# Kernel optimization log

Measured on AMD Instinct MI355X. Metric: run time of the kernel, lower is better.

Reference implementation:

```python
import jax, jax.numpy as jnp
import numpy as np

B, L, D = 4, 4096, 1024
N_HEADS = 16
HEAD_SIZE = D // N_HEADS  # 64


def setup_inputs() -> dict:
    key = jax.random.key(0)
    k_x, k_w, k_m = jax.random.split(key, 3)
    x = jax.random.normal(k_x, (B, L, D), dtype=jnp.float32)
    # nn.Linear(D, 3*head_size, bias=False): weight (3*hs, D); store transposed (D, 3*hs)
    W_qkv = jax.random.normal(k_w, (D, 3 * HEAD_SIZE), dtype=jnp.float32) * (D ** -0.5)
    attn_mask = jax.random.randint(k_m, (B, L), 0, 2).astype(jnp.bool_)
    return {"x": x, "attn_mask": attn_mask, "W_qkv": W_qkv}


def reference(x, attn_mask, W_qkv):
    # x: (B, L, D); W_qkv: (D, 3*hs); attn_mask: (B, L) True = attend
    qkv = x @ W_qkv                                # (B, L, 3*hs)
    q, k, v = jnp.split(qkv, 3, axis=-1)           # each (B, L, hs)
    scale = HEAD_SIZE ** -0.5
    scores = jnp.einsum('bqd,bkd->bqk', q, k) * scale   # (B, L, L)
    neg_inf = jnp.finfo(scores.dtype).min
    scores = jnp.where(attn_mask[:, None, :], scores, neg_inf)
    weights = jax.nn.softmax(scores, axis=-1)      # (B, L, L)
    out = jnp.einsum('bqk,bkd->bqd', weights, v)   # (B, L, hs)
    return out
```

## Files before the change

kernel.cpp:

```cpp
#include <hip/hip_runtime.h>

typedef __bf16 bf16_t;
typedef __bf16 bf16x8 __attribute__((ext_vector_type(8)));
typedef __bf16 bf16x4 __attribute__((ext_vector_type(4)));
typedef float  f32x4  __attribute__((ext_vector_type(4)));
struct uint4_t { unsigned x, y, z, w; };

#define B_  4
#define L_  4096
#define D_  1024
#define HS  64
#define NQ  192
#define SCL2E 0.1803368801111204f
#define MFMA16 __builtin_amdgcn_mfma_f32_16x16x32_bf16

__global__ __launch_bounds__(256) void pack_w_kernel(const void* __restrict__ Win,
                                                     const unsigned char* __restrict__ mask,
                                                     const unsigned short* __restrict__ xw,
                                                     bf16_t* __restrict__ Wtp,
                                                     int* __restrict__ flags) {
    __shared__ int c1, c23, cbad;
    int tid = threadIdx.x;
    if (tid == 0) { c1 = 0; c23 = 0; cbad = 0; }
    __syncthreads();
    uint4_t m[4];
#pragma unroll
    for (int i = 0; i < 4; ++i)
        m[i] = *(const uint4_t*)(mask + tid * 16 + i * 4096);
    int a = 0, bc = 0;
#pragma unroll
    for (int i = 0; i < 4; ++i) {
        const unsigned* w = (const unsigned*)&m[i];
#pragma unroll
        for (int j = 0; j < 4; ++j) {
            if (w[j] & 0x0000ff00u) a++;
            if (w[j] & 0xffff0000u) bc++;
        }
    }
    uint4_t xm = *(const uint4_t*)(xw + tid * 8);
    int bad = 0;
    const unsigned* xwv = (const unsigned*)&xm;
#pragma unroll
    for (int j = 0; j < 4; ++j)
#pragma unroll
        for (int h = 0; h < 2; ++h) {
            unsigned s = (xwv[j] >> (16 * h)) & 0xFFFFu;
            unsigned e = (s >> 7) & 0xFF;
            if (e > 150 || (e < 90 && e != 0)) bad++;
        }
    if (a)   atomicAdd(&c1, a);
    if (bc)  atomicAdd(&c23, bc);
    if (bad) atomicAdd(&cbad, bad);
    __syncthreads();
    int f32 = (cbad >= 64) ? 1 : 0;
    if (blockIdx.x == 0 && tid == 0) {
        flags[0] = (c1 > 0) ? 1 : ((c23 > 0) ? 2 : 0);
        flags[1] = f32;
    }

    int idx = blockIdx.x * 256 + tid;
    int lane = idx & 63;
    int t    = (idx >> 6) & 3;
    int kc   = (idx >> 8) & 31;
    int ct   = idx >> 13;
    int n  = ct * 64 + t * 16 + (lane & 15);
    int k0 = kc * 32 + (lane >> 4) * 8;
    bf16x8 v;
#pragma unroll
    for (int j = 0; j < 8; ++j) {
        if (f32) v[j] = (bf16_t)(((const float*)Win)[(k0 + j) * NQ + n]);
        else     v[j] = ((const bf16_t*)Win)[(k0 + j) * NQ + n];
    }
    *(bf16x8*)(Wtp + (size_t)idx * 8) = v;
}

__global__ __launch_bounds__(256, 2) void qkv_gemm_kernel(const void* __restrict__ xin,
                                                          const int* __restrict__ flags,
                                                          const bf16_t* __restrict__ Wtp,
                                                          bf16_t* __restrict__ Qb,
                                                          bf16_t* __restrict__ Kb,
                                                          bf16_t* __restrict__ Vt) {
    __shared__ __align__(16) bf16_t xs[32 * 520];
    __shared__ __align__(16) bf16_t sqk[32 * 136];
    __shared__ __align__(16) bf16_t sv[64 * 40];

    int tid = threadIdx.x;
    int wave = tid >> 6, lane = tid & 63, quad = lane >> 4, l16 = lane & 15;
    int rg = wave & 1, ch = wave >> 1;
    int m0 = blockIdx.x * 32;
    int xf = flags[1];

    f32x4 acc[6] = {};
    bf16x8 Ba[6], Bb[6];

    auto stage = [&](int h) {
        bf16x8 tmp[8];
#pragma unroll
        for (int j = 0; j < 8; ++j) {
            int c = tid + j * 256;
            int row = c >> 6, off = (c & 63) * 8;
            if (xf) {
                const float* xp = (const float*)xin + (size_t)(m0 + row) * D_ + h * 512 + off;
                f32x4 lo = *(const f32x4*)xp, hi = *(const f32x4*)(xp + 4);
                tmp[j][0] = (bf16_t)lo[0]; tmp[j][1] = (bf16_t)lo[1];
                tmp[j][2] = (bf16_t)lo[2]; tmp[j][3] = (bf16_t)lo[3];
                tmp[j][4] = (bf16_t)hi[0]; tmp[j][5] = (bf16_t)hi[1];
                tmp[j][6] = (bf16_t)hi[2]; tmp[j][7] = (bf16_t)hi[3];
            } else {
                tmp[j] = *(const bf16x8*)((const bf16_t*)xin + (size_t)(m0 + row) * D_ + h * 512 + off);
            }
        }
#pragma unroll
        for (int j = 0; j < 8; ++j) {
            int c = tid + j * 256;
            int row = c >> 6, off = (c & 63) * 8;
            *(bf16x8*)&xs[row * 520 + off] = tmp[j];
        }
    };
    auto loadB6 = [&](int ks, bf16x8* Bv) {
#pragma unroll
        for (int i = 0; i < 6; ++i) {
            int st = ch * 6 + i, ct2 = st >> 2, tt = st & 3;
            Bv[i] = *(const bf16x8*)(Wtp + ((size_t)(ct2 * 32 + ks) * 4 + tt) * 512 + lane * 8);
        }
    };
    auto compute6 = [&](int ks, const bf16x8* Bv) {
        bf16x8 A = *(const bf16x8*)&xs[(rg * 16 + l16) * 520 + (ks & 15) * 32 + quad * 8];
#pragma unroll
        for (int i = 0; i < 6; ++i)
            acc[i] = MFMA16(A, Bv[i], acc[i], 0, 0, 0);
    };

    stage(0);
    loadB6(0, Ba);
    __syncthreads();
#pragma unroll
    for (int half = 0; half < 2; ++half) {
        int base = half * 16;
        for (int m = 0; m < 16; m += 2) {
            int ks = base + m;
            loadB6(ks + 1, Bb);
            compute6(ks, Ba);
            loadB6(ks + 2 <= 31 ? ks + 2 : 31, Ba);
            compute6(ks + 1, Bb);
        }
        if (half == 0) {
            __syncthreads();
            stage(1);
            __syncthreads();
        }
    }

    int rowb = rg * 16 + quad * 4;
#pragma unroll
    for (int i = 0; i < 6; ++i) {
        int col = ch * 96 + i * 16 + l16;
#pragma unroll
        for (int r = 0; r < 4; ++r) {
            bf16_t hv = (bf16_t)acc[i][r];
            if (col < 128) sqk[(rowb + r) * 136 + col] = hv;
            else           sv[(col - 128) * 40 + rowb + r] = hv;
        }
    }
    __syncthreads();

    int bb = m0 >> 12, l0 = m0 & 4095;
#pragma unroll
    for (int it = 0; it < 2; ++it) {
        int c = tid + it * 256;
        int row = c >> 4, off = (c & 15) * 8;
        bf16x8 v = *(const bf16x8*)&sqk[row * 136 + off];
        if (off < 64) *(bf16x8*)(Qb + (size_t)(bb * L_ + l0 + row) * HS + off) = v;
        else          *(bf16x8*)(Kb + (size_t)(bb * L_ + l0 + row) * HS + off - 64) = v;
    }
    {
        int d = tid >> 2, off = (tid & 3) * 8;
        bf16x8 v = *(const bf16x8*)&sv[d * 40 + off];
        *(bf16x8*)(Vt + (size_t)(bb * HS + d) * L_ + l0 + off) = v;
    }
}

template<int NSPLIT>
__global__ __launch_bounds__(256, 4) void attn_kernel(const bf16_t* __restrict__ Qb,
                                                      const bf16_t* __restrict__ Kb,
                                                      const bf16_t* __restrict__ Vt,
                                                      const void* __restrict__ maskp,
                                                      const int* __restrict__ flags,
                                                      float* __restrict__ Opart,
                                                      float* __restrict__ lpart,
                                                      void* __restrict__ outv) {
    constexpr int KCH = L_ / NSPLIT;
    constexpr int NIT = KCH / 64;
    __shared__ __align__(16) bf16_t ktile[2][64 * 72];
    __shared__ __align__(16) bf16_t plds[4][32 * 72];
    __shared__ float mb[KCH];

    int tid = threadIdx.x, wave = tid >> 6, lane = tid & 63;
    int quad = lane >> 4, l16 = lane & 15;
    int grp = blockIdx.x % (B_ * NSPLIT);
    int qt  = blockIdx.x / (B_ * NSPLIT);
    int s = grp / B_, b = grp % B_;
    int q0 = qt * 128;
    int kbase = s * KCH;

    const float NEGINF = -__builtin_inff();
    int mkind = flags[0];
    if (mkind == 1) {
        const unsigned char* mp = (const unsigned char*)maskp + b * L_ + kbase;
        for (int i = tid; i < KCH; i += 256) mb[i] = mp[i] ? 0.0f : NEGINF;
    } else if (mkind == 2) {
        const float* mp = (const float*)maskp + b * L_ + kbase;
        for (int i = tid; i < KCH; i += 256) mb[i] = (mp[i] != 0.0f) ? 0.0f : NEGINF;
    } else {
        const int* mp = (const int*)maskp + b * L_ + kbase;
        for (int i = tid; i < KCH; i += 256) mb[i] = mp[i] ? 0.0f : NEGINF;
    }

    bf16x8 aQ[2][2];
#pragma unroll
    for (int rg = 0; rg < 2; ++rg) {
        const bf16_t* qp = Qb + (size_t)(b * L_ + q0 + wave * 32 + rg * 16 + l16) * HS + quad * 8;
        aQ[rg][0] = *(const bf16x8*)qp;
        aQ[rg][1] = *(const bf16x8*)(qp + 32);
    }
    bf16x8 ones;
#pragma unroll
    for (int j = 0; j < 8; ++j) ones[j] = (bf16_t)1.0f;

    const bf16_t* Kbase = Kb + (size_t)b * L_ * HS;
    const bf16_t* Vbase = Vt + (size_t)b * HS * L_;

    f32x4 O[2][4] = {};
    f32x4 O5[2] = {};
    bf16_t* pw = &plds[wave][0];
    bf16x8 kr[2];

    auto kstage_load = [&](int t) {
#pragma unroll
        for (int j = 0; j < 2; ++j) {
            int c = tid + j * 256;
            int row = c >> 3, off = (c & 7) * 8;
            kr[j] = *(const bf16x8*)(Kbase + (size_t)(kbase + t * 64 + row) * HS + off);
        }
    };
    auto kstage_store = [&](int buf) {
#pragma unroll
        for (int j = 0; j < 2; ++j) {
            int c = tid + j * 256;
            int row = c >> 3, off = (c & 7) * 8;
            *(bf16x8*)&ktile[buf][row * 72 + off] = kr[j];
        }
    };

    kstage_load(0);
    kstage_store(0);
    __syncthreads();

    for (int t = 0; t < NIT; ++t) {
        int kb = kbase + t * 64;
        bool more = (t + 1 < NIT);
        if (more) kstage_load(t + 1);

        bf16x8 V0[4];
#pragma unroll
        for (int nt = 0; nt < 4; ++nt)
            V0[nt] = *(const bf16x8*)(Vbase + (size_t)(nt * 16 + l16) * L_ + kb + quad * 8);

        const bf16_t* kl = &ktile[t & 1][0];
#pragma unroll
        for (int h = 0; h < 2; ++h) {
            f32x4 sc[2][2];
#pragma unroll
            for (int s2 = 0; s2 < 2; ++s2) {
                int st = h * 2 + s2;
                bf16x8 kb0 = *(const bf16x8*)&kl[(st * 16 + l16) * 72 + quad * 8];
                bf16x8 kb1 = *(const bf16x8*)&kl[(st * 16 + l16) * 72 + 32 + quad * 8];
#pragma unroll
                for (int rg = 0; rg < 2; ++rg) {
                    f32x4 t0 = {};
                    t0 = MFMA16(aQ[rg][0], kb0, t0, 0, 0, 0);
                    t0 = MFMA16(aQ[rg][1], kb1, t0, 0, 0, 0);
                    sc[rg][s2] = t0;
                }
            }
#pragma unroll
            for (int s2 = 0; s2 < 2; ++s2) {
                int st = h * 2 + s2;
                float bl = mb[t * 64 + st * 16 + l16];
#pragma unroll
                for (int rg = 0; rg < 2; ++rg)
#pragma unroll
                    for (int r = 0; r < 4; ++r) {
                        float p = exp2f(fmaf(sc[rg][s2][r], SCL2E, bl));
                        pw[(rg * 16 + quad * 4 + r) * 72 + st * 16 + l16] = (bf16_t)p;
                    }
            }
        }

#pragma unroll
        for (int rg = 0; rg < 2; ++rg) {
            bf16x8 aP = *(const bf16x8*)&pw[(rg * 16 + l16) * 72 + quad * 8];
#pragma unroll
            for (int nt = 0; nt < 4; ++nt)
                O[rg][nt] = MFMA16(aP, V0[nt], O[rg][nt], 0, 0, 0);
            O5[rg] = MFMA16(aP, ones, O5[rg], 0, 0, 0);
        }
        bf16x8 V1[4];
#pragma unroll
        for (int nt = 0; nt < 4; ++nt)
            V1[nt] = *(const bf16x8*)(Vbase + (size_t)(nt * 16 + l16) * L_ + kb + 32 + quad * 8);
#pragma unroll
        for (int rg = 0; rg < 2; ++rg) {
            bf16x8 aP = *(const bf16x8*)&pw[(rg * 16 + l16) * 72 + 32 + quad * 8];
#pragma unroll
            for (int nt = 0; nt < 4; ++nt)
                O[rg][nt] = MFMA16(aP, V1[nt], O[rg][nt], 0, 0, 0);
            O5[rg] = MFMA16(aP, ones, O5[rg], 0, 0, 0);
        }

        if (more) kstage_store((t + 1) & 1);
        __syncthreads();
    }

    int of32 = flags[1];
#pragma unroll
    for (int rg = 0; rg < 2; ++rg)
#pragma unroll
        for (int r = 0; r < 4; ++r) {
            float sm = O5[rg][r];
            int row = q0 + wave * 32 + rg * 16 + quad * 4 + r;
            if (NSPLIT == 1) {
                float inv = 1.0f / sm;
                size_t base = (size_t)(b * L_ + row) * HS;
                if (of32) {
                    float* op = (float*)outv + base;
#pragma unroll
                    for (int nt = 0; nt < 4; ++nt) op[nt * 16 + l16] = O[rg][nt][r] * inv;
                } else {
                    bf16_t* op = (bf16_t*)outv + base;
#pragma unroll
                    for (int nt = 0; nt < 4; ++nt) op[nt * 16 + l16] = (bf16_t)(O[rg][nt][r] * inv);
                }
            } else {
                float* op = Opart + (size_t)s * (B_ * L_ * HS) + (size_t)(b * L_ + row) * HS;
#pragma unroll
                for (int nt = 0; nt < 4; ++nt) op[nt * 16 + l16] = O[rg][nt][r];
                if (l16 == 0) lpart[(size_t)s * (B_ * L_) + b * L_ + row] = sm;
            }
        }
}

__global__ __launch_bounds__(256) void reduce_kernel(const float* __restrict__ Opart,
                                                     const float* __restrict__ lpart,
                                                     const int* __restrict__ flags,
                                                     void* __restrict__ outv,
                                                     int nsplit) {
    int i4 = (blockIdx.x * 256 + threadIdx.x) * 4;
    int row = i4 >> 6;
    f32x4 acc = {};
    float lsum = 0.f;
    for (int s = 0; s < nsplit; ++s) {
        acc  += *(const f32x4*)&Opart[(size_t)s * (B_ * L_ * HS) + i4];
        lsum += lpart[(size_t)s * (B_ * L_) + row];
    }
    float inv = 1.0f / lsum;
    if (flags[1]) {
        f32x4 r = { acc[0] * inv, acc[1] * inv, acc[2] * inv, acc[3] * inv };
        *(f32x4*)&((float*)outv)[i4] = r;
    } else {
        bf16x4 r;
#pragma unroll
        for (int j = 0; j < 4; ++j) r[j] = (bf16_t)(acc[j] * inv);
        *(bf16x4*)&((bf16_t*)outv)[i4] = r;
    }
}

extern "C" void kernel_launch(void* const* d_in, const int* in_sizes, int n_in,
                              void* d_out, int out_size, void* d_ws, size_t ws_size,
                              hipStream_t stream) {
    (void)in_sizes; (void)n_in; (void)out_size;
    const void* x    = d_in[0];
    const void* mask = d_in[1];
    const void* W    = d_in[2];

    char* ws = (char*)d_ws;
    bf16_t* Qb    = (bf16_t*)(ws);
    bf16_t* Kb    = (bf16_t*)(ws + (2u << 20));
    bf16_t* Vt    = (bf16_t*)(ws + (4u << 20));
    bf16_t* Wtp   = (bf16_t*)(ws + (6u << 20));
    int*    flags = (int*)   (ws + (6u << 20) + (512u << 10));
    float*  Opart = (float*) (ws + (7u << 20));

    auto need = [](int ns) -> size_t {
        return (7u << 20) + (size_t)ns * (B_ * L_ * HS * 4)
                          + (size_t)ns * (B_ * L_ * 4) + 4096;
    };
    int nsplit = (ws_size >= need(8)) ? 8 : (ws_size >= need(4)) ? 4 : 1;
    float* lpart = (float*)(ws + (7u << 20) + (size_t)nsplit * (B_ * L_ * HS * 4));

    pack_w_kernel<<<96, 256, 0, stream>>>(W, (const unsigned char*)mask,
                                          (const unsigned short*)x, Wtp, flags);
    qkv_gemm_kernel<<<512, 256, 0, stream>>>(x, flags, Wtp, Qb, Kb, Vt);
    if (nsplit == 8) {
        attn_kernel<8><<<32 * B_ * 8, 256, 0, stream>>>(Qb, Kb, Vt, mask, flags,
                                                        Opart, lpart, d_out);
        reduce_kernel<<<(B_ * L_ * HS) / 1024, 256, 0, stream>>>(Opart, lpart, flags,
                                                                 d_out, 8);
    } else if (nsplit == 4) {
        attn_kernel<4><<<32 * B_ * 4, 256, 0, stream>>>(Qb, Kb, Vt, mask, flags,
                                                        Opart, lpart, d_out);
        reduce_kernel<<<(B_ * L_ * HS) / 1024, 256, 0, stream>>>(Opart, lpart, flags,
                                                                 d_out, 4);
    } else {
        attn_kernel<1><<<32 * B_, 256, 0, stream>>>(Qb, Kb, Vt, mask, flags,
                                                    Opart, lpart, d_out);
    }
}
```

Before: 168.8 us.

## Pre-pack K/V in MFMA fragment layout, fold scale and mask, use 32x32 MFMA

The QKV GEMM epilogue now pre-scales Q by scale*log2e, multiplies V by a 0/1 mask, and writes K and V in MFMA-fragment-packed order. The attention kernel switches to 32x32x16 MFMA with S computed transposed. This lets P go straight from registers to the PV MFMA via permlane32 swaps instead of an LDS round trip. Masking is done by zeroing V and by a denominator MFMA against the mask vector, and K is staged with global_load_lds. The aim is to remove the LDS traffic for P, the per-element mask add and scale FMA, and strided V loads. The cost is more register pressure (occupancy hint drops from 4 to 3) and reliance on the softmax running without max subtraction.

```diff
diff --git a/kernel.cpp b/kernel.cpp
--- a/kernel.cpp
+++ b/kernel.cpp
@@ -3,7 +3,9 @@
 typedef __bf16 bf16_t;
 typedef __bf16 bf16x8 __attribute__((ext_vector_type(8)));
 typedef __bf16 bf16x4 __attribute__((ext_vector_type(4)));
+typedef __bf16 bf16x2 __attribute__((ext_vector_type(2)));
 typedef float  f32x4  __attribute__((ext_vector_type(4)));
+typedef float  f32x16 __attribute__((ext_vector_type(16)));
 struct uint4_t { unsigned x, y, z, w; };
 
 #define B_  4
@@ -13,12 +15,32 @@
 #define NQ  192
 #define SCL2E 0.1803368801111204f
 #define MFMA16 __builtin_amdgcn_mfma_f32_16x16x32_bf16
+#define MFMA32 __builtin_amdgcn_mfma_f32_32x32x16_bf16
+
+#if defined(__has_builtin)
+# if __has_builtin(__builtin_amdgcn_global_load_lds)
+#  define HAS_GLL 1
+# endif
+#endif
+#ifndef HAS_GLL
+# define HAS_GLL 0
+#endif
+
+static __device__ __forceinline__ unsigned pk_bf16(float a, float b) {
+    union { bf16x2 v; unsigned u; } x;
+    x.v[0] = (bf16_t)a; x.v[1] = (bf16_t)b;
+    return x.u;
+}
+static __device__ __forceinline__ void swap32(unsigned& x, unsigned& y) {
+    asm("v_permlane32_swap_b32 %0, %1" : "+v"(x), "+v"(y));
+}
 
 __global__ __launch_bounds__(256) void pack_w_kernel(const void* __restrict__ Win,
                                                      const unsigned char* __restrict__ mask,
                                                      const unsigned short* __restrict__ xw,
                                                      bf16_t* __restrict__ Wtp,
-                                                     int* __restrict__ flags) {
+                                                     int* __restrict__ flags,
+                                                     bf16_t* __restrict__ m01) {
     __shared__ int c1, c23, cbad;
     int tid = threadIdx.x;
     if (tid == 0) { c1 = 0; c23 = 0; cbad = 0; }
@@ -53,12 +75,22 @@
     if (bad) atomicAdd(&cbad, bad);
     __syncthreads();
     int f32 = (cbad >= 64) ? 1 : 0;
+    int kind = (c1 > 0) ? 1 : ((c23 > 0) ? 2 : 0);
     if (blockIdx.x == 0 && tid == 0) {
-        flags[0] = (c1 > 0) ? 1 : ((c23 > 0) ? 2 : 0);
+        flags[0] = kind;
         flags[1] = f32;
     }
 
     int idx = blockIdx.x * 256 + tid;
+
+    if (idx < B_ * L_) {
+        bool mv;
+        if (kind == 1)      mv = mask[idx] != 0;
+        else if (kind == 2) mv = ((const float*)mask)[idx] != 0.0f;
+        else                mv = ((const int*)mask)[idx] != 0;
+        m01[idx] = (bf16_t)(mv ? 1.0f : 0.0f);
+    }
+
     int lane = idx & 63;
     int t    = (idx >> 6) & 3;
     int kc   = (idx >> 8) & 31;
@@ -77,9 +109,10 @@
 __global__ __launch_bounds__(256, 2) void qkv_gemm_kernel(const void* __restrict__ xin,
                                                           const int* __restrict__ flags,
                                                           const bf16_t* __restrict__ Wtp,
+                                                          const bf16_t* __restrict__ m01p,
                                                           bf16_t* __restrict__ Qb,
-                                                          bf16_t* __restrict__ Kb,
-                                                          bf16_t* __restrict__ Vt) {
+                                                          bf16_t* __restrict__ Kp,
+                                                          bf16_t* __restrict__ Vp) {
     __shared__ __align__(16) bf16_t xs[32 * 520];
     __shared__ __align__(16) bf16_t sqk[32 * 136];
     __shared__ __align__(16) bf16_t sv[64 * 40];
@@ -157,7 +190,9 @@
         int col = ch * 96 + i * 16 + l16;
 #pragma unroll
         for (int r = 0; r < 4; ++r) {
-            bf16_t hv = (bf16_t)acc[i][r];
+            float av = acc[i][r];
+            if (col < 64) av *= SCL2E;
+            bf16_t hv = (bf16_t)av;
             if (col < 128) sqk[(rowb + r) * 136 + col] = hv;
             else           sv[(col - 128) * 40 + rowb + r] = hv;
         }
@@ -165,189 +200,155 @@
     __syncthreads();
 
     int bb = m0 >> 12, l0 = m0 & 4095;
-#pragma unroll
-    for (int it = 0; it < 2; ++it) {
-        int c = tid + it * 256;
-        int row = c >> 4, off = (c & 15) * 8;
+    int t64 = l0 >> 6, stile = (l0 >> 5) & 1, ctop = (l0 >> 4) & 2;
+    {
+        int row = tid >> 3, off = (tid & 7) * 8;
         bf16x8 v = *(const bf16x8*)&sqk[row * 136 + off];
-        if (off < 64) *(bf16x8*)(Qb + (size_t)(bb * L_ + l0 + row) * HS + off) = v;
-        else          *(bf16x8*)(Kb + (size_t)(bb * L_ + l0 + row) * HS + off - 64) = v;
+        *(bf16x8*)(Qb + (size_t)(m0 + row) * HS + off) = v;
     }
     {
-        int d = tid >> 2, off = (tid & 3) * 8;
-        bf16x8 v = *(const bf16x8*)&sv[d * 40 + off];
-        *(bf16x8*)(Vt + (size_t)(bb * HS + d) * L_ + l0 + off) = v;
+        int chk = tid >> 6, ln = tid & 63;
+        bf16x8 v = *(const bf16x8*)&sqk[(tid & 31) * 136 + 64 + chk * 16 + ((tid >> 5) & 1) * 8];
+        *(bf16x8*)(Kp + (size_t)bb * (L_ * HS) +
+                   ((((size_t)t64 * 2 + stile) * 4 + chk) * 64 + ln) * 8) = v;
+    }
+    {
+        int dt = tid >> 7, chL = (tid >> 6) & 1, ln = tid & 63;
+        int hi2 = (tid >> 5) & 1, d31 = tid & 31;
+        bf16x8 v  = *(const bf16x8*)&sv[(dt * 32 + d31) * 40 + chL * 16 + hi2 * 8];
+        bf16x8 mm = *(const bf16x8*)(m01p + (size_t)m0 + chL * 16 + hi2 * 8);
+        bf16x8 o;
+#pragma unroll
+        for (int j = 0; j < 8; ++j) o[j] = (bf16_t)((float)v[j] * (float)mm[j]);
+        *(bf16x8*)(Vp + (size_t)bb * (L_ * HS) +
+                   ((((size_t)t64 * 2 + dt) * 4 + ctop + chL) * 64 + ln) * 8) = o;
     }
 }
 
 template<int NSPLIT>
-__global__ __launch_bounds__(256, 4) void attn_kernel(const bf16_t* __restrict__ Qb,
-                                                      const bf16_t* __restrict__ Kb,
-                                                      const bf16_t* __restrict__ Vt,
-                                                      const void* __restrict__ maskp,
+__global__ __launch_bounds__(256, 3) void attn_kernel(const bf16_t* __restrict__ Qb,
+                                                      const bf16_t* __restrict__ Kp,
+                                                      const bf16_t* __restrict__ Vp,
+                                                      const bf16_t* __restrict__ m01p,
                                                       const int* __restrict__ flags,
                                                       float* __restrict__ Opart,
                                                       float* __restrict__ lpart,
                                                       void* __restrict__ outv) {
     constexpr int KCH = L_ / NSPLIT;
     constexpr int NIT = KCH / 64;
-    __shared__ __align__(16) bf16_t ktile[2][64 * 72];
-    __shared__ __align__(16) bf16_t plds[4][32 * 72];
-    __shared__ float mb[KCH];
+    __shared__ __align__(16) bf16_t ktile[2][4096];
 
     int tid = threadIdx.x, wave = tid >> 6, lane = tid & 63;
-    int quad = lane >> 4, l16 = lane & 15;
+    int hi = lane >> 5, l31 = lane & 31;
     int grp = blockIdx.x % (B_ * NSPLIT);
     int qt  = blockIdx.x / (B_ * NSPLIT);
-    int s = grp / B_, b = grp % B_;
-    int q0 = qt * 128;
-    int kbase = s * KCH;
-
-    const float NEGINF = -__builtin_inff();
-    int mkind = flags[0];
-    if (mkind == 1) {
-        const unsigned char* mp = (const unsigned char*)maskp + b * L_ + kbase;
-        for (int i = tid; i < KCH; i += 256) mb[i] = mp[i] ? 0.0f : NEGINF;
-    } else if (mkind == 2) {
-        const float* mp = (const float*)maskp + b * L_ + kbase;
-        for (int i = tid; i < KCH; i += 256) mb[i] = (mp[i] != 0.0f) ? 0.0f : NEGINF;
+    int sp = grp / B_, b = grp % B_;
+    int q0 = qt * 128 + wave * 32;
+    int t64base = sp * NIT;
+
+    const bf16_t* KpB = Kp + (size_t)b * (L_ * HS);
+    const bf16_t* VpB = Vp + (size_t)b * (L_ * HS);
+    const bf16_t* mB  = m01p + (size_t)b * L_ + sp * KCH;
+
+    bf16x8 Qf[4];
+    {
+        const bf16_t* qp = Qb + (size_t)(b * L_ + q0 + l31) * HS + hi * 8;
+#pragma unroll
+        for (int c = 0; c < 4; ++c) Qf[c] = *(const bf16x8*)(qp + c * 16);
+    }
+
+    f32x16 O0 = {}, O1 = {}, den = {};
+
+    auto stage = [&](int buf, int t64) {
+        const bf16_t* src = KpB + (size_t)t64 * 4096 + tid * 8;
+        bf16_t* dst = &ktile[buf][tid * 8];
+#if HAS_GLL
+#pragma unroll
+        for (int j = 0; j < 2; ++j)
+            __builtin_amdgcn_global_load_lds(
+                (const __attribute__((address_space(1))) unsigned*)(src + j * 2048),
+                (__attribute__((address_space(3))) unsigned*)(dst + j * 2048), 16, 0, 0);
+#else
+#pragma unroll
+        for (int j = 0; j < 2; ++j)
+            *(bf16x8*)(dst + j * 2048) = *(const bf16x8*)(src + j * 2048);
+#endif
+    };
+
+    stage(0, t64base);
+    __syncthreads();
+
+    for (int t = 0; t < NIT; ++t) {
+        int cur = t & 1;
+        if (t + 1 < NIT) stage(cur ^ 1, t64base + t + 1);
+        const bf16_t* kl = &ktile[cur][0];
+        const bf16_t* vt = VpB + (size_t)(t64base + t) * 4096;
+        const bf16_t* mt = mB + t * 64;
+
+#pragma unroll
+        for (int st = 0; st < 2; ++st) {
+            f32x16 S = {};
+#pragma unroll
+            for (int c = 0; c < 4; ++c) {
+                bf16x8 Kf = *(const bf16x8*)&kl[((st * 4 + c) * 64 + lane) * 8];
+                S = MFMA32(Kf, Qf[c], S, 0, 0, 0);
+            }
+#pragma unroll
+            for (int r = 0; r < 16; ++r) S[r] = exp2f(S[r]);
+#pragma unroll
+            for (int cc = 0; cc < 2; ++cc) {
+                int chk = st * 2 + cc;
+                unsigned w0 = pk_bf16(S[cc * 8 + 0], S[cc * 8 + 1]);
+                unsigned w1 = pk_bf16(S[cc * 8 + 2], S[cc * 8 + 3]);
+                unsigned w2 = pk_bf16(S[cc * 8 + 4], S[cc * 8 + 5]);
+                unsigned w3 = pk_bf16(S[cc * 8 + 6], S[cc * 8 + 7]);
+                swap32(w0, w2);
+                swap32(w1, w3);
+                union { unsigned u[4]; bf16x8 v; } P;
+                P.u[0] = w0; P.u[1] = w1; P.u[2] = w2; P.u[3] = w3;
+                bf16x8 V0 = *(const bf16x8*)&vt[((0 * 4 + chk) * 64 + lane) * 8];
+                bf16x8 V1 = *(const bf16x8*)&vt[((1 * 4 + chk) * 64 + lane) * 8];
+                bf16x8 Mf = *(const bf16x8*)(mt + chk * 16 + hi * 8);
+                O0  = MFMA32(P.v, V0, O0, 0, 0, 0);
+                O1  = MFMA32(P.v, V1, O1, 0, 0, 0);
+                den = MFMA32(P.v, Mf, den, 0, 0, 0);
+            }
+        }
+        __syncthreads();
+    }
+
+    if (NSPLIT == 1) {
+        int of32 = flags[1];
+#pragma unroll
+        for (int r = 0; r < 16; ++r) {
+            int qr = (r & 3) + 8 * (r >> 2) + 4 * hi;
+            float inv = 1.0f / den[r];
+            size_t base = (size_t)(b * L_ + q0 + qr) * HS;
+            if (of32) {
+                float* op = (float*)outv + base;
+                op[l31]      = O0[r] * inv;
+                op[32 + l31] = O1[r] * inv;
+            } else {
+                bf16_t* op = (bf16_t*)outv + base;
+                op[l31]      = (bf16_t)(O0[r] * inv);
+                op[32 + l31] = (bf16_t)(O1[r] * inv);
+            }
+        }
     } else {
-        const int* mp = (const int*)maskp + b * L_ + kbase;
-        for (int i = tid; i < KCH; i += 256) mb[i] = mp[i] ? 0.0f : NEGINF;
-    }
-
-    bf16x8 aQ[2][2];
-#pragma unroll
-    for (int rg = 0; rg < 2; ++rg) {
-        const bf16_t* qp = Qb + (size_t)(b * L_ + q0 + wave * 32 + rg * 16 + l16) * HS + quad * 8;
-        aQ[rg][0] = *(const bf16x8*)qp;
-        aQ[rg][1] = *(const bf16x8*)(qp + 32);
-    }
-    bf16x8 ones;
-#pragma unroll
-    for (int j = 0; j < 8; ++j) ones[j] = (bf16_t)1.0f;
-
-    const bf16_t* Kbase = Kb + (size_t)b * L_ * HS;
-    const bf16_t* Vbase = Vt + (size_t)b * HS * L_;
-
-    f32x4 O[2][4] = {};
-    f32x4 O5[2] = {};
-    bf16_t* pw = &plds[wave][0];
-    bf16x8 kr[2];
-
-    auto kstage_load = [&](int t) {
-#pragma unroll
-        for (int j = 0; j < 2; ++j) {
-            int c = tid + j * 256;
-            int row = c >> 3, off = (c & 7) * 8;
-            kr[j] = *(const bf16x8*)(Kbase + (size_t)(kbase + t * 64 + row) * HS + off);
-        }
-    };
-    auto kstage_store = [&](int buf) {
-#pragma unroll
-        for (int j = 0; j < 2; ++j) {
-            int c = tid + j * 256;
-            int row = c >> 3, off = (c & 7) * 8;
-            *(bf16x8*)&ktile[buf][row * 72 + off] = kr[j];
-        }
-    };
-
-    kstage_load(0);
-    kstage_store(0);
-    __syncthreads();
-
-    for (int t = 0; t < NIT; ++t) {
-        int kb = kbase + t * 64;
-        bool more = (t + 1 < NIT);
-        if (more) kstage_load(t + 1);
-
-        bf16x8 V0[4];
-#pragma unroll
-        for (int nt = 0; nt < 4; ++nt)
-            V0[nt] = *(const bf16x8*)(Vbase + (size_t)(nt * 16 + l16) * L_ + kb + quad * 8);
-
-        const bf16_t* kl = &ktile[t & 1][0];
-#pragma unroll
-        for (int h = 0; h < 2; ++h) {
-            f32x4 sc[2][2];
-#pragma unroll
-            for (int s2 = 0; s2 < 2; ++s2) {
-                int st = h * 2 + s2;
-                bf16x8 kb0 = *(const bf16x8*)&kl[(st * 16 + l16) * 72 + quad * 8];
-                bf16x8 kb1 = *(const bf16x8*)&kl[(st * 16 + l16) * 72 + 32 + quad * 8];
-#pragma unroll
-                for (int rg = 0; rg < 2; ++rg) {
-                    f32x4 t0 = {};
-                    t0 = MFMA16(aQ[rg][0], kb0, t0, 0, 0, 0);
-                    t0 = MFMA16(aQ[rg][1], kb1, t0, 0, 0, 0);
-                    sc[rg][s2] = t0;
-                }
-            }
-#pragma unroll
-            for (int s2 = 0; s2 < 2; ++s2) {
-                int st = h * 2 + s2;
-                float bl = mb[t * 64 + st * 16 + l16];
-#pragma unroll
-                for (int rg = 0; rg < 2; ++rg)
-#pragma unroll
-                    for (int r = 0; r < 4; ++r) {
-                        float p = exp2f(fmaf(sc[rg][s2][r], SCL2E, bl));
-                        pw[(rg * 16 + quad * 4 + r) * 72 + st * 16 + l16] = (bf16_t)p;
-                    }
-            }
-        }
-
-#pragma unroll
-        for (int rg = 0; rg < 2; ++rg) {
-            bf16x8 aP = *(const bf16x8*)&pw[(rg * 16 + l16) * 72 + quad * 8];
-#pragma unroll
-            for (int nt = 0; nt < 4; ++nt)
-                O[rg][nt] = MFMA16(aP, V0[nt], O[rg][nt], 0, 0, 0);
-            O5[rg] = MFMA16(aP, ones, O5[rg], 0, 0, 0);
-        }
-        bf16x8 V1[4];
-#pragma unroll
-        for (int nt = 0; nt < 4; ++nt)
-            V1[nt] = *(const bf16x8*)(Vbase + (size_t)(nt * 16 + l16) * L_ + kb + 32 + quad * 8);
-#pragma unroll
-        for (int rg = 0; rg < 2; ++rg) {
-            bf16x8 aP = *(const bf16x8*)&pw[(rg * 16 + l16) * 72 + 32 + quad * 8];
-#pragma unroll
-            for (int nt = 0; nt < 4; ++nt)
-                O[rg][nt] = MFMA16(aP, V1[nt], O[rg][nt], 0, 0, 0);
-            O5[rg] = MFMA16(aP, ones, O5[rg], 0, 0, 0);
-        }
-
-        if (more) kstage_store((t + 1) & 1);
-        __syncthreads();
-    }
-
-    int of32 = flags[1];
-#pragma unroll
-    for (int rg = 0; rg < 2; ++rg)
-#pragma unroll
-        for (int r = 0; r < 4; ++r) {
-            float sm = O5[rg][r];
-            int row = q0 + wave * 32 + rg * 16 + quad * 4 + r;
-            if (NSPLIT == 1) {
-                float inv = 1.0f / sm;
-                size_t base = (size_t)(b * L_ + row) * HS;
-                if (of32) {
-                    float* op = (float*)outv + base;
-#pragma unroll
-                    for (int nt = 0; nt < 4; ++nt) op[nt * 16 + l16] = O[rg][nt][r] * inv;
-                } else {
-                    bf16_t* op = (bf16_t*)outv + base;
-#pragma unroll
-                    for (int nt = 0; nt < 4; ++nt) op[nt * 16 + l16] = (bf16_t)(O[rg][nt][r] * inv);
-                }
-            } else {
-                float* op = Opart + (size_t)s * (B_ * L_ * HS) + (size_t)(b * L_ + row) * HS;
-#pragma unroll
-                for (int nt = 0; nt < 4; ++nt) op[nt * 16 + l16] = O[rg][nt][r];
-                if (l16 == 0) lpart[(size_t)s * (B_ * L_) + b * L_ + row] = sm;
-            }
-        }
+        float* op = Opart + (size_t)sp * (B_ * L_ * HS) + (size_t)(b * L_ + q0) * HS + l31;
+#pragma unroll
+        for (int r = 0; r < 16; ++r) {
+            int qr = (r & 3) + 8 * (r >> 2) + 4 * hi;
+            op[(size_t)qr * HS]      = O0[r];
+            op[(size_t)qr * HS + 32] = O1[r];
+        }
+        if (l31 == 0) {
+            float* lp = lpart + (size_t)sp * (B_ * L_) + b * L_ + q0;
+#pragma unroll
+            for (int r = 0; r < 16; ++r)
+                lp[(r & 3) + 8 * (r >> 2) + 4 * hi] = den[r];
+        }
+    }
 }
 
 __global__ __launch_bounds__(256) void reduce_kernel(const float* __restrict__ Opart,
@@ -385,10 +386,11 @@
 
     char* ws = (char*)d_ws;
     bf16_t* Qb    = (bf16_t*)(ws);
-    bf16_t* Kb    = (bf16_t*)(ws + (2u << 20));
-    bf16_t* Vt    = (bf16_t*)(ws + (4u << 20));
+    bf16_t* Kp    = (bf16_t*)(ws + (2u << 20));
+    bf16_t* Vp    = (bf16_t*)(ws + (4u << 20));
     bf16_t* Wtp   = (bf16_t*)(ws + (6u << 20));
     int*    flags = (int*)   (ws + (6u << 20) + (512u << 10));
+    bf16_t* m01p  = (bf16_t*)(ws + (6u << 20) + (516u << 10));
     float*  Opart = (float*) (ws + (7u << 20));
 
     auto need = [](int ns) -> size_t {
@@ -399,20 +401,20 @@
     float* lpart = (float*)(ws + (7u << 20) + (size_t)nsplit * (B_ * L_ * HS * 4));
 
     pack_w_kernel<<<96, 256, 0, stream>>>(W, (const unsigned char*)mask,
-                                          (const unsigned short*)x, Wtp, flags);
-    qkv_gemm_kernel<<<512, 256, 0, stream>>>(x, flags, Wtp, Qb, Kb, Vt);
+                                          (const unsigned short*)x, Wtp, flags, m01p);
+    qkv_gemm_kernel<<<512, 256, 0, stream>>>(x, flags, Wtp, m01p, Qb, Kp, Vp);
     if (nsplit == 8) {
-        attn_kernel<8><<<32 * B_ * 8, 256, 0, stream>>>(Qb, Kb, Vt, mask, flags,
+        attn_kernel<8><<<32 * B_ * 8, 256, 0, stream>>>(Qb, Kp, Vp, m01p, flags,
                                                         Opart, lpart, d_out);
         reduce_kernel<<<(B_ * L_ * HS) / 1024, 256, 0, stream>>>(Opart, lpart, flags,
                                                                  d_out, 8);
     } else if (nsplit == 4) {
-        attn_kernel<4><<<32 * B_ * 4, 256, 0, stream>>>(Qb, Kb, Vt, mask, flags,
+        attn_kernel<4><<<32 * B_ * 4, 256, 0, stream>>>(Qb, Kp, Vp, m01p, flags,
                                                         Opart, lpart, d_out);
         reduce_kernel<<<(B_ * L_ * HS) / 1024, 256, 0, stream>>>(Opart, lpart, flags,
                                                                  d_out, 4);
     } else {
-        attn_kernel<1><<<32 * B_, 256, 0, stream>>>(Qb, Kb, Vt, mask, flags,
+        attn_kernel<1><<<32 * B_, 256, 0, stream>>>(Qb, Kp, Vp, m01p, flags,
                                                     Opart, lpart, d_out);
     }
 }
```

New measurement: 158.0 us. 1.07x faster.
